# Performance work log

Measured on AMD Instinct MI355X. Metric: run time of the kernel, lower is better.

Reference implementation:

```python
import jax, jax.numpy as jnp
import numpy as np

DIM = 256
NUM_HEADS = 8
SCALE = (DIM // NUM_HEADS) ** (-0.5)
EPS = 1e-6


def channel_layernorm(x, w, b):
    # LayerNorm over channel dim (axis=1) per spatial location, as in source
    u = jnp.mean(x, axis=1, keepdims=True)
    s = jnp.mean((x - u) ** 2, axis=1, keepdims=True)
    xn = (x - u) / jnp.sqrt(s + EPS)
    return w[:, None, None] * xn + b[:, None, None]


def conv1x1(x, W, b):
    # x: [B,C,H,W], W: [O,C], b: [O]
    return jnp.einsum('bchw,oc->bohw', x, W) + b[:, None, None]


def setup_inputs() -> dict:
    key = jax.random.key(0)
    ks = jax.random.split(key, 10)
    B, C, H, W = 8, DIM, 48, 48
    inp = {
        'x1': jax.random.normal(ks[0], (B, C, H, W), jnp.float32),
        'x2': jax.random.normal(ks[1], (B, C, H, W), jnp.float32),
        'Wq': jax.random.normal(ks[2], (C, C), jnp.float32) * (1.0 / np.sqrt(C)),
        'bq': jnp.zeros((C,), jnp.float32),
        'Wk': jax.random.normal(ks[3], (C, C), jnp.float32) * (1.0 / np.sqrt(C)),
        'bk': jnp.zeros((C,), jnp.float32),
        'Wv': jax.random.normal(ks[4], (C, C), jnp.float32) * (1.0 / np.sqrt(C)),
        'bv': jnp.zeros((C,), jnp.float32),
        'Wp': jax.random.normal(ks[5], (C, C), jnp.float32) * (1.0 / np.sqrt(C)),
        'bp': jnp.zeros((C,), jnp.float32),
        'w_nq': jnp.ones((C,), jnp.float32),
        'b_nq': jnp.zeros((C,), jnp.float32),
        'w_nkv': jnp.ones((C,), jnp.float32),
        'b_nkv': jnp.zeros((C,), jnp.float32),
    }
    return inp


def reference(x1, x2, Wq, bq, Wk, bk, Wv, bv, Wp, bp, w_nq, b_nq, w_nkv, b_nkv):
    B, C, H, W = x1.shape
    x1n = channel_layernorm(x1, w_nq, b_nq)
    x2n = channel_layernorm(x2, w_nkv, b_nkv)
    # project then flatten spatial -> tokens: [B, N, C]
    q = conv1x1(x1n, Wq, bq).reshape(B, C, H * W).transpose(0, 2, 1)
    k = conv1x1(x2n, Wk, bk).reshape(B, C, H * W).transpose(0, 2, 1)
    v = conv1x1(x2n, Wv, bv).reshape(B, C, H * W).transpose(0, 2, 1)
    # single-head full attention over N tokens (heads never split in source)
    attn = jnp.einsum('bnc,bmc->bnm', q, k) * SCALE
    attn = jax.nn.softmax(attn, axis=-1)
    out = jnp.einsum('bnm,bmc->bnc', attn, v)  # [B,N,C]
    out = out.transpose(0, 2, 1).reshape(B, C, H, W)
    out = conv1x1(out, Wp, bp)
    return out + x1
```

## Files before the change

kernel.cpp:

```cpp
#include <hip/hip_runtime.h>

#define NB 8
#define CH 256
#define NT 2304
#define KVSPLIT 3
#define TPS 12
#define ATTN_SCALE 0.17677669529663687f
#define LN_EPS 1e-6f

typedef __attribute__((ext_vector_type(8))) short short8;
typedef __attribute__((ext_vector_type(4))) float f32x4;
typedef __attribute__((ext_vector_type(4))) unsigned short ushort4v;
typedef __attribute__((ext_vector_type(8))) unsigned short ushort8v;
typedef __attribute__((ext_vector_type(4))) float float4v;

__device__ __forceinline__ unsigned short f2bf(float f) {
  unsigned int u = __float_as_uint(f);
  u += 0x7fffu + ((u >> 16) & 1u);
  return (unsigned short)(u >> 16);
}
__device__ __forceinline__ float bf2f(unsigned short s) {
  return __uint_as_float(((unsigned int)s) << 16);
}

__device__ __forceinline__ void gload_lds16(const void* g, void* l) {
  __builtin_amdgcn_global_load_lds(
      (const __attribute__((address_space(1))) unsigned int*)g,
      (__attribute__((address_space(3))) unsigned int*)l, 16, 0, 0);
}

__global__ __launch_bounds__(256) void wconv_kernel(
    const float* __restrict__ wq, const float* __restrict__ wk,
    const float* __restrict__ wv, const float* __restrict__ wp,
    unsigned short* __restrict__ out) {
  int z = blockIdx.y;
  const float* src = (z == 0) ? wq : (z == 1) ? wk : (z == 2) ? wv : wp;
  unsigned short* dst = out + z * 65536;
  int i = (blockIdx.x * 256 + threadIdx.x) * 4;
  float4v v = *(const float4v*)(src + i);
  ushort4v r;
  r[0] = f2bf(v[0]); r[1] = f2bf(v[1]); r[2] = f2bf(v[2]); r[3] = f2bf(v[3]);
  *(ushort4v*)(dst + i) = r;
}

__global__ __launch_bounds__(256) void ln_kernel(
    const float* __restrict__ x1, const float* __restrict__ x2,
    const float* __restrict__ w1, const float* __restrict__ b1,
    const float* __restrict__ w2, const float* __restrict__ b2,
    unsigned short* __restrict__ o1, unsigned short* __restrict__ o2) {
  __shared__ float part[4][64][2];
  __shared__ float fin[64][2];
  int z = blockIdx.z;
  const float* x = z ? x2 : x1;
  const float* w = z ? w2 : w1;
  const float* bias = z ? b2 : b1;
  unsigned short* out = z ? o2 : o1;
  int tid = threadIdx.x;
  int lane = tid & 63, wv = tid >> 6;
  int n0 = blockIdx.x * 64;
  int b = blockIdx.y;
  const float* xp = x + (size_t)b * CH * NT + n0 + lane;
  float sum = 0.f, ss = 0.f;
#pragma unroll 4
  for (int c = wv * 64; c < wv * 64 + 64; ++c) {
    float v = xp[(size_t)c * NT];
    sum += v; ss += v * v;
  }
  part[wv][lane][0] = sum;
  part[wv][lane][1] = ss;
  __syncthreads();
  if (tid < 64) {
    float s = 0.f, q = 0.f;
#pragma unroll
    for (int wi = 0; wi < 4; ++wi) { s += part[wi][tid][0]; q += part[wi][tid][1]; }
    float u = s * (1.0f / CH);
    float var = q * (1.0f / CH) - u * u;
    fin[tid][0] = u;
    fin[tid][1] = rsqrtf(var + LN_EPS);
  }
  __syncthreads();
  float u = fin[lane][0], rstd = fin[lane][1];
  unsigned short* op = out + ((size_t)b * NT + n0 + lane) * CH;
  for (int c0 = wv * 64; c0 < wv * 64 + 64; c0 += 8) {
    ushort8v pk;
#pragma unroll
    for (int j = 0; j < 8; ++j) {
      float v = xp[(size_t)(c0 + j) * NT];
      pk[j] = f2bf((v - u) * rstd * w[c0 + j] + bias[c0 + j]);
    }
    *(ushort8v*)(op + c0) = pk;
  }
}

__global__ __launch_bounds__(256) void proj_kernel(
    const unsigned short* __restrict__ xq, const unsigned short* __restrict__ xkv,
    const unsigned short* __restrict__ wbf,
    const float* __restrict__ bq, const float* __restrict__ bk,
    const float* __restrict__ bv,
    unsigned short* __restrict__ q, unsigned short* __restrict__ k,
    unsigned short* __restrict__ vt) {
  __shared__ char As[16384];
  __shared__ char Bs[16384];
  int tid = threadIdx.x;
  int lane = tid & 63, wid = tid >> 6;
  int z = blockIdx.z;
  int b = z / 3, pz = z - b * 3;
  const unsigned short* A = ((pz == 0) ? xq : xkv) + (size_t)b * NT * CH;
  const unsigned short* W = wbf + pz * 65536;
  const float* bias = (pz == 0) ? bq : (pz == 1) ? bk : bv;
  int m0 = blockIdx.x * 128;
  int c0 = blockIdx.y * 128;
  int wr = wid >> 1, wc = wid & 1;

  f32x4 zero4 = {0.f, 0.f, 0.f, 0.f};
  f32x4 acc[4][4];
#pragma unroll
  for (int i = 0; i < 4; ++i)
#pragma unroll
    for (int j = 0; j < 4; ++j) acc[i][j] = zero4;

  for (int kt = 0; kt < 4; ++kt) {
#pragma unroll
    for (int it = 0; it < 4; ++it) {
      int li = it * 256 + tid;
      int X = li * 16;
      int row = X >> 7;
      int colb = (X & 127) ^ ((row & 7) << 4);
      gload_lds16((const char*)A + ((size_t)(m0 + row) * CH + kt * 64) * 2 + colb,
                  As + it * 4096 + wid * 1024);
      gload_lds16((const char*)W + ((size_t)(c0 + row) * CH + kt * 64) * 2 + colb,
                  Bs + it * 4096 + wid * 1024);
    }
    __syncthreads();
#pragma unroll
    for (int kk = 0; kk < 2; ++kk) {
      int cb = kk * 64 + ((lane >> 4) << 4);
      short8 af[4], bf[4];
#pragma unroll
      for (int mi = 0; mi < 4; ++mi) {
        int row = wr * 64 + mi * 16 + (lane & 15);
        af[mi] = *(const short8*)(As + row * 128 + (cb ^ ((row & 7) << 4)));
      }
#pragma unroll
      for (int ni = 0; ni < 4; ++ni) {
        int row = wc * 64 + ni * 16 + (lane & 15);
        bf[ni] = *(const short8*)(Bs + row * 128 + (cb ^ ((row & 7) << 4)));
      }
#pragma unroll
      for (int mi = 0; mi < 4; ++mi)
#pragma unroll
        for (int ni = 0; ni < 4; ++ni)
          acc[mi][ni] = __builtin_amdgcn_mfma_f32_16x16x32_bf16(
              af[mi], bf[ni], acc[mi][ni], 0, 0, 0);
    }
    __syncthreads();
  }

  int colbase = c0 + wc * 64;
  int rowbase = m0 + wr * 64;
  if (pz < 2) {
    unsigned short* dst = ((pz == 0) ? q : k) + (size_t)b * NT * CH;
#pragma unroll
    for (int mi = 0; mi < 4; ++mi)
#pragma unroll
      for (int ni = 0; ni < 4; ++ni) {
        int col = colbase + ni * 16 + (lane & 15);
        float bb = bias[col];
        int row0 = rowbase + mi * 16 + ((lane >> 4) << 2);
#pragma unroll
        for (int r = 0; r < 4; ++r)
          dst[(size_t)(row0 + r) * CH + col] = f2bf(acc[mi][ni][r] + bb);
      }
  } else {
    unsigned short* dst = vt + (size_t)b * CH * NT;
#pragma unroll
    for (int mi = 0; mi < 4; ++mi)
#pragma unroll
      for (int ni = 0; ni < 4; ++ni) {
        int col = colbase + ni * 16 + (lane & 15);
        float bb = bias[col];
        int row0 = rowbase + mi * 16 + ((lane >> 4) << 2);
        ushort4v pk;
#pragma unroll
        for (int r = 0; r < 4; ++r) pk[r] = f2bf(acc[mi][ni][r] + bb);
        *(ushort4v*)(dst + (size_t)col * NT + row0) = pk;
      }
  }
}

__global__ __launch_bounds__(256, 2) void attn_kernel(
    const unsigned short* __restrict__ q, const unsigned short* __restrict__ k,
    const unsigned short* __restrict__ vt,
    unsigned short* __restrict__ op0, unsigned short* __restrict__ op1,
    unsigned short* __restrict__ op2, float* __restrict__ ml) {
  __shared__ char Ks[2][32768];
  __shared__ char Ps[9216];
  __shared__ float Alf[64];
  int tid = threadIdx.x, lane = tid & 63, wid = tid >> 6;
  int b = blockIdx.z;
  int split = blockIdx.y;
  int q0 = blockIdx.x * 64;
  const unsigned short* qb = q + (size_t)b * NT * CH;
  const unsigned short* kb = k + (size_t)b * NT * CH;
  const unsigned short* vb = vt + (size_t)b * CH * NT;
  int hi = lane >> 4, lo = lane & 15;

  short8 qf[8];
  int qrow = q0 + wid * 16 + lo;
#pragma unroll
  for (int ks = 0; ks < 8; ++ks)
    qf[ks] = *(const short8*)(qb + (size_t)qrow * CH + ks * 32 + hi * 8);

  f32x4 zero4 = {0.f, 0.f, 0.f, 0.f};
  f32x4 o[16];
#pragma unroll
  for (int ci = 0; ci < 16; ++ci) o[ci] = zero4;
  float mrun = -INFINITY, lrun = 0.f;

  int kt0base = split * TPS * 64;
#pragma unroll
  for (int it = 0; it < 8; ++it) {
    int X = (it * 256 + tid) * 16;
    int row = X >> 9;
    int colb = (X & 511) ^ ((row & 7) << 4);
    gload_lds16((const char*)kb + ((size_t)(kt0base + row) * CH) * 2 + colb,
                Ks[0] + it * 4096 + wid * 1024);
  }
  __syncthreads();

  for (int t = 0; t < TPS; ++t) {
    int kt0 = kt0base + t * 64;
    int cur = t & 1;
    if (t + 1 < TPS) {
#pragma unroll
      for (int it = 0; it < 8; ++it) {
        int X = (it * 256 + tid) * 16;
        int row = X >> 9;
        int colb = (X & 511) ^ ((row & 7) << 4);
        gload_lds16((const char*)kb + ((size_t)(kt0 + 64 + row) * CH) * 2 + colb,
                    Ks[cur ^ 1] + it * 4096 + wid * 1024);
      }
    }
    short8 vf[8];
#pragma unroll
    for (int di = 0; di < 4; ++di)
#pragma unroll
      for (int ks2 = 0; ks2 < 2; ++ks2)
        vf[di * 2 + ks2] = *(const short8*)(
            vb + (size_t)(wid * 64 + di * 16 + lo) * NT + kt0 + ks2 * 32 + hi * 8);

    f32x4 s[4];
#pragma unroll
    for (int ct = 0; ct < 4; ++ct) s[ct] = zero4;
#pragma unroll
    for (int ct = 0; ct < 4; ++ct) {
      int row = ct * 16 + lo;
      const char* kp = Ks[cur] + row * 512;
      int swz = (row & 7) << 4;
#pragma unroll
      for (int ks = 0; ks < 8; ++ks) {
        short8 kf = *(const short8*)(kp + ((ks * 64 + hi * 16) ^ swz));
        s[ct] = __builtin_amdgcn_mfma_f32_16x16x32_bf16(kf, qf[ks], s[ct], 0, 0, 0);
      }
    }

    float mx = -INFINITY;
#pragma unroll
    for (int ct = 0; ct < 4; ++ct) {
      f32x4 sv = s[ct] * ATTN_SCALE;
      s[ct] = sv;
      mx = fmaxf(fmaxf(fmaxf(mx, sv[0]), fmaxf(sv[1], sv[2])), sv[3]);
    }
    mx = fmaxf(mx, __shfl_xor(mx, 16));
    mx = fmaxf(mx, __shfl_xor(mx, 32));
    float mnew = fmaxf(mrun, mx);
    float alpha = __expf(mrun - mnew);
    mrun = mnew;
    float rs = 0.f;
    unsigned short* prow = (unsigned short*)(Ps + (wid * 16 + lo) * 144 + hi * 8);
#pragma unroll
    for (int ct = 0; ct < 4; ++ct) {
      ushort4v pk;
#pragma unroll
      for (int r = 0; r < 4; ++r) {
        float p = __expf(s[ct][r] - mnew);
        rs += p;
        pk[r] = f2bf(p);
      }
      *(ushort4v*)(prow + ct * 16) = pk;
    }
    rs += __shfl_xor(rs, 16);
    rs += __shfl_xor(rs, 32);
    lrun = lrun * alpha + rs;
    if (lane < 16) Alf[wid * 16 + lane] = alpha;
    __syncthreads();

    f32x4 af[4];
#pragma unroll
    for (int qg = 0; qg < 4; ++qg)
      af[qg] = *(const f32x4*)(Alf + qg * 16 + hi * 4);
#pragma unroll
    for (int qg = 0; qg < 4; ++qg)
#pragma unroll
      for (int di = 0; di < 4; ++di) o[qg * 4 + di] *= af[qg];

#pragma unroll
    for (int ks2 = 0; ks2 < 2; ++ks2) {
      short8 pa[4];
#pragma unroll
      for (int qg = 0; qg < 4; ++qg)
        pa[qg] = *(const short8*)(Ps + (qg * 16 + lo) * 144 + ks2 * 64 + hi * 16);
#pragma unroll
      for (int di = 0; di < 4; ++di)
#pragma unroll
        for (int qg = 0; qg < 4; ++qg)
          o[qg * 4 + di] = __builtin_amdgcn_mfma_f32_16x16x32_bf16(
              pa[qg], vf[di * 2 + ks2], o[qg * 4 + di], 0, 0, 0);
    }
    __syncthreads();
  }

  unsigned short* od = ((split == 0) ? op0 : (split == 1) ? op1 : op2) +
                       ((size_t)b * NT + q0) * CH;
#pragma unroll
  for (int qg = 0; qg < 4; ++qg)
#pragma unroll
    for (int di = 0; di < 4; ++di) {
      int d = wid * 64 + di * 16 + lo;
#pragma unroll
      for (int r = 0; r < 4; ++r) {
        int qr = qg * 16 + hi * 4 + r;
        od[(size_t)qr * CH + d] = f2bf(o[qg * 4 + di][r]);
      }
    }
  float* mlp = ml + ((size_t)(split * NB + b) * NT + q0) * 2;
  if (lane < 16) {
    int qr = wid * 16 + lane;
    mlp[qr * 2] = mrun;
    mlp[qr * 2 + 1] = lrun;
  }
}

__global__ __launch_bounds__(256) void combine_kernel(
    const unsigned short* __restrict__ op0, const unsigned short* __restrict__ op1,
    const unsigned short* __restrict__ op2, const float* __restrict__ ml,
    unsigned short* __restrict__ oa) {
  int g = blockIdx.x;
  int d = threadIdx.x;
  const size_t S = (size_t)NB * NT;
  float m0 = ml[(size_t)g * 2], l0 = ml[(size_t)g * 2 + 1];
  float m1 = ml[(S + g) * 2], l1 = ml[(S + g) * 2 + 1];
  float m2 = ml[(2 * S + g) * 2], l2 = ml[(2 * S + g) * 2 + 1];
  float M = fmaxf(fmaxf(m0, m1), m2);
  float w0 = __expf(m0 - M), w1 = __expf(m1 - M), w2 = __expf(m2 - M);
  float L = w0 * l0 + w1 * l1 + w2 * l2;
  float o0 = bf2f(op0[(size_t)g * CH + d]);
  float o1 = bf2f(op1[(size_t)g * CH + d]);
  float o2 = bf2f(op2[(size_t)g * CH + d]);
  oa[(size_t)g * CH + d] = f2bf((w0 * o0 + w1 * o1 + w2 * o2) / L);
}

__global__ __launch_bounds__(256) void oproj_kernel(
    const unsigned short* __restrict__ oa, const unsigned short* __restrict__ wp,
    const float* __restrict__ bp, const float* __restrict__ x1,
    float* __restrict__ outp) {
  __shared__ char As[16384];
  __shared__ char Bs[16384];
  int tid = threadIdx.x;
  int lane = tid & 63, wid = tid >> 6;
  int b = blockIdx.z;
  const unsigned short* A = oa + (size_t)b * NT * CH;
  int m0 = blockIdx.x * 128;
  int c0 = blockIdx.y * 128;
  int wr = wid >> 1, wc = wid & 1;

  f32x4 zero4 = {0.f, 0.f, 0.f, 0.f};
  f32x4 acc[4][4];
#pragma unroll
  for (int i = 0; i < 4; ++i)
#pragma unroll
    for (int j = 0; j < 4; ++j) acc[i][j] = zero4;

  for (int kt = 0; kt < 4; ++kt) {
#pragma unroll
    for (int it = 0; it < 4; ++it) {
      int li = it * 256 + tid;
      int X = li * 16;
      int row = X >> 7;
      int colb = (X & 127) ^ ((row & 7) << 4);
      gload_lds16((const char*)A + ((size_t)(m0 + row) * CH + kt * 64) * 2 + colb,
                  As + it * 4096 + wid * 1024);
      gload_lds16((const char*)wp + ((size_t)(c0 + row) * CH + kt * 64) * 2 + colb,
                  Bs + it * 4096 + wid * 1024);
    }
    __syncthreads();
#pragma unroll
    for (int kk = 0; kk < 2; ++kk) {
      int cb = kk * 64 + ((lane >> 4) << 4);
      short8 af[4], bf[4];
#pragma unroll
      for (int mi = 0; mi < 4; ++mi) {
        int row = wr * 64 + mi * 16 + (lane & 15);
        af[mi] = *(const short8*)(As + row * 128 + (cb ^ ((row & 7) << 4)));
      }
#pragma unroll
      for (int ni = 0; ni < 4; ++ni) {
        int row = wc * 64 + ni * 16 + (lane & 15);
        bf[ni] = *(const short8*)(Bs + row * 128 + (cb ^ ((row & 7) << 4)));
      }
#pragma unroll
      for (int mi = 0; mi < 4; ++mi)
#pragma unroll
        for (int ni = 0; ni < 4; ++ni)
          acc[mi][ni] = __builtin_amdgcn_mfma_f32_16x16x32_bf16(
              af[mi], bf[ni], acc[mi][ni], 0, 0, 0);
    }
    __syncthreads();
  }

  int colbase = c0 + wc * 64;
  int rowbase = m0 + wr * 64;
#pragma unroll
  for (int mi = 0; mi < 4; ++mi)
#pragma unroll
    for (int ni = 0; ni < 4; ++ni) {
      int col = colbase + ni * 16 + (lane & 15);
      float bb = bp[col];
      int row0 = rowbase + mi * 16 + ((lane >> 4) << 2);
      int base = (b * CH + col) * NT + row0;
      float4v xv = *(const float4v*)(x1 + base);
      float4v rs;
#pragma unroll
      for (int r = 0; r < 4; ++r) rs[r] = acc[mi][ni][r] + bb + xv[r];
      *(float4v*)(outp + base) = rs;
    }
}

extern "C" void kernel_launch(void* const* d_in, const int* in_sizes, int n_in,
                              void* d_out, int out_size, void* d_ws, size_t ws_size,
                              hipStream_t stream) {
  (void)in_sizes; (void)n_in; (void)out_size; (void)ws_size;
  const float* x1 = (const float*)d_in[0];
  const float* x2 = (const float*)d_in[1];
  const float* Wq = (const float*)d_in[2];
  const float* bq = (const float*)d_in[3];
  const float* Wk = (const float*)d_in[4];
  const float* bk = (const float*)d_in[5];
  const float* Wv = (const float*)d_in[6];
  const float* bv = (const float*)d_in[7];
  const float* Wp = (const float*)d_in[8];
  const float* bp = (const float*)d_in[9];
  const float* wnq = (const float*)d_in[10];
  const float* bnq = (const float*)d_in[11];
  const float* wnkv = (const float*)d_in[12];
  const float* bnkv = (const float*)d_in[13];
  float* outp = (float*)d_out;

  const size_t TSZ = (size_t)NB * NT * CH;
  unsigned short* xq = (unsigned short*)d_ws;
  unsigned short* xkv = xq + TSZ;
  unsigned short* qb = xkv + TSZ;
  unsigned short* kbuf = qb + TSZ;
  unsigned short* vtb = kbuf + TSZ;
  unsigned short* oab = vtb + TSZ;
  unsigned short* wbf = oab + TSZ;
  float* ml = (float*)(wbf + 4 * 65536);

  wconv_kernel<<<dim3(64, 4), dim3(256), 0, stream>>>(Wq, Wk, Wv, Wp, wbf);
  ln_kernel<<<dim3(36, 8, 2), dim3(256), 0, stream>>>(x1, x2, wnq, bnq, wnkv, bnkv,
                                                      xq, xkv);
  proj_kernel<<<dim3(18, 2, 24), dim3(256), 0, stream>>>(xq, xkv, wbf, bq, bk, bv,
                                                         qb, kbuf, vtb);
  attn_kernel<<<dim3(36, KVSPLIT, 8), dim3(256), 0, stream>>>(qb, kbuf, vtb,
                                                              xq, xkv, oab, ml);
  combine_kernel<<<dim3(NB * NT), dim3(256), 0, stream>>>(xq, xkv, oab, ml, oab);
  oproj_kernel<<<dim3(18, 2, 8), dim3(256), 0, stream>>>(oab, wbf + 3 * 65536, bp,
                                                         x1, outp);
}
```

Before: 158.4 us.

## Rewrite attention with 32x32 MFMA, register-resident P, lazy rescale, vectorized combine

The attention kernel now handles 128 queries per block, with each wave owning 32 query rows. It uses 32x32x16 bf16 MFMA and keeps the softmax probabilities in registers, converted with v_cvt_pk_bf16_f32, so the LDS P buffer and the alpha-exchange barrier are gone. The attention scale moves into the Q projection, and the running-max rescale only happens when the max grows by more than 8, which relies on bf16/fp32 headroom. The LN kernel also caches the input column in registers instead of reading x twice, and the combine kernel is vectorized to 8 elements per thread with a precomputed reciprocal. The cost is higher register pressure in attention, and the deferred max may reduce accuracy.

Result: slower. 316.3 us (+99.7%).

```diff
diff --git a/kernel.cpp b/kernel.cpp
--- a/kernel.cpp
+++ b/kernel.cpp
@@ -5,11 +5,13 @@
 #define NT 2304
 #define KVSPLIT 3
 #define TPS 12
+#define QB 128
 #define ATTN_SCALE 0.17677669529663687f
 #define LN_EPS 1e-6f
 
 typedef __attribute__((ext_vector_type(8))) short short8;
 typedef __attribute__((ext_vector_type(4))) float f32x4;
+typedef __attribute__((ext_vector_type(16))) float f32x16;
 typedef __attribute__((ext_vector_type(4))) unsigned short ushort4v;
 typedef __attribute__((ext_vector_type(8))) unsigned short ushort8v;
 typedef __attribute__((ext_vector_type(4))) float float4v;
@@ -21,6 +23,11 @@
 }
 __device__ __forceinline__ float bf2f(unsigned short s) {
   return __uint_as_float(((unsigned int)s) << 16);
+}
+__device__ __forceinline__ unsigned int cvtpk(float a, float b) {
+  unsigned int r;
+  asm("v_cvt_pk_bf16_f32 %0, %1, %2" : "=v"(r) : "v"(a), "v"(b));
+  return r;
 }
 
 __device__ __forceinline__ void gload_lds16(const void* g, void* l) {
@@ -60,10 +67,12 @@
   int n0 = blockIdx.x * 64;
   int b = blockIdx.y;
   const float* xp = x + (size_t)b * CH * NT + n0 + lane;
+  float xc[64];
   float sum = 0.f, ss = 0.f;
-#pragma unroll 4
-  for (int c = wv * 64; c < wv * 64 + 64; ++c) {
-    float v = xp[(size_t)c * NT];
+#pragma unroll
+  for (int j = 0; j < 64; ++j) {
+    float v = xp[(size_t)(wv * 64 + j) * NT];
+    xc[j] = v;
     sum += v; ss += v * v;
   }
   part[wv][lane][0] = sum;
@@ -81,14 +90,14 @@
   __syncthreads();
   float u = fin[lane][0], rstd = fin[lane][1];
   unsigned short* op = out + ((size_t)b * NT + n0 + lane) * CH;
-  for (int c0 = wv * 64; c0 < wv * 64 + 64; c0 += 8) {
+#pragma unroll
+  for (int c0 = 0; c0 < 64; c0 += 8) {
     ushort8v pk;
 #pragma unroll
-    for (int j = 0; j < 8; ++j) {
-      float v = xp[(size_t)(c0 + j) * NT];
-      pk[j] = f2bf((v - u) * rstd * w[c0 + j] + bias[c0 + j]);
-    }
-    *(ushort8v*)(op + c0) = pk;
+    for (int j = 0; j < 8; ++j)
+      pk[j] = f2bf((xc[c0 + j] - u) * rstd * w[wv * 64 + c0 + j] +
+                   bias[wv * 64 + c0 + j]);
+    *(ushort8v*)(op + wv * 64 + c0) = pk;
   }
 }
 
@@ -160,6 +169,7 @@
   int rowbase = m0 + wr * 64;
   if (pz < 2) {
     unsigned short* dst = ((pz == 0) ? q : k) + (size_t)b * NT * CH;
+    float scl = (pz == 0) ? ATTN_SCALE : 1.0f;
 #pragma unroll
     for (int mi = 0; mi < 4; ++mi)
 #pragma unroll
@@ -169,7 +179,7 @@
         int row0 = rowbase + mi * 16 + ((lane >> 4) << 2);
 #pragma unroll
         for (int r = 0; r < 4; ++r)
-          dst[(size_t)(row0 + r) * CH + col] = f2bf(acc[mi][ni][r] + bb);
+          dst[(size_t)(row0 + r) * CH + col] = f2bf((acc[mi][ni][r] + bb) * scl);
       }
   } else {
     unsigned short* dst = vt + (size_t)b * CH * NT;
@@ -194,27 +204,24 @@
     unsigned short* __restrict__ op0, unsigned short* __restrict__ op1,
     unsigned short* __restrict__ op2, float* __restrict__ ml) {
   __shared__ char Ks[2][32768];
-  __shared__ char Ps[9216];
-  __shared__ float Alf[64];
   int tid = threadIdx.x, lane = tid & 63, wid = tid >> 6;
+  int r31 = lane & 31, h2 = lane >> 5;
   int b = blockIdx.z;
   int split = blockIdx.y;
-  int q0 = blockIdx.x * 64;
-  const unsigned short* qb = q + (size_t)b * NT * CH;
+  int q0 = blockIdx.x * QB;
+  const unsigned short* qb_ = q + (size_t)b * NT * CH;
   const unsigned short* kb = k + (size_t)b * NT * CH;
-  const unsigned short* vb = vt + (size_t)b * CH * NT;
-  int hi = lane >> 4, lo = lane & 15;
-
-  short8 qf[8];
-  int qrow = q0 + wid * 16 + lo;
-#pragma unroll
-  for (int ks = 0; ks < 8; ++ks)
-    qf[ks] = *(const short8*)(qb + (size_t)qrow * CH + ks * 32 + hi * 8);
-
-  f32x4 zero4 = {0.f, 0.f, 0.f, 0.f};
-  f32x4 o[16];
-#pragma unroll
-  for (int ci = 0; ci < 16; ++ci) o[ci] = zero4;
+  const unsigned short* vbase = vt + (size_t)b * CH * NT + (size_t)r31 * NT;
+
+  int qrow = q0 + wid * 32 + r31;
+  short8 qf[16];
+#pragma unroll
+  for (int st = 0; st < 16; ++st)
+    qf[st] = *(const short8*)(qb_ + (size_t)qrow * CH + st * 16 + h2 * 8);
+
+  f32x16 o[8];
+#pragma unroll
+  for (int i = 0; i < 8; ++i) o[i] = (f32x16){};
   float mrun = -INFINITY, lrun = 0.f;
 
   int kt0base = split * TPS * 64;
@@ -228,9 +235,12 @@
   }
   __syncthreads();
 
+  union V8 { struct { ushort4v a, b; } h; short8 s8; };
+  union PB { unsigned int u[4]; short8 s8; };
+
   for (int t = 0; t < TPS; ++t) {
     int kt0 = kt0base + t * 64;
-    int cur = t & 1;
+    const char* kbase = Ks[t & 1];
     if (t + 1 < TPS) {
 #pragma unroll
       for (int it = 0; it < 8; ++it) {
@@ -238,106 +248,106 @@
         int row = X >> 9;
         int colb = (X & 511) ^ ((row & 7) << 4);
         gload_lds16((const char*)kb + ((size_t)(kt0 + 64 + row) * CH) * 2 + colb,
-                    Ks[cur ^ 1] + it * 4096 + wid * 1024);
-      }
-    }
-    short8 vf[8];
-#pragma unroll
-    for (int di = 0; di < 4; ++di)
-#pragma unroll
-      for (int ks2 = 0; ks2 < 2; ++ks2)
-        vf[di * 2 + ks2] = *(const short8*)(
-            vb + (size_t)(wid * 64 + di * 16 + lo) * NT + kt0 + ks2 * 32 + hi * 8);
-
-    f32x4 s[4];
-#pragma unroll
-    for (int ct = 0; ct < 4; ++ct) s[ct] = zero4;
-#pragma unroll
-    for (int ct = 0; ct < 4; ++ct) {
-      int row = ct * 16 + lo;
-      const char* kp = Ks[cur] + row * 512;
-      int swz = (row & 7) << 4;
-#pragma unroll
-      for (int ks = 0; ks < 8; ++ks) {
-        short8 kf = *(const short8*)(kp + ((ks * 64 + hi * 16) ^ swz));
-        s[ct] = __builtin_amdgcn_mfma_f32_16x16x32_bf16(kf, qf[ks], s[ct], 0, 0, 0);
-      }
-    }
+                    Ks[(t + 1) & 1] + it * 4096 + wid * 1024);
+      }
+    }
+
+    f32x16 s0 = (f32x16){}, s1 = (f32x16){};
+    __builtin_amdgcn_s_setprio(1);
+#pragma unroll
+    for (int st = 0; st < 16; ++st) {
+      int cb = (st * 32 + h2 * 16);
+      short8 kf0 = *(const short8*)(kbase + r31 * 512 + (cb ^ ((r31 & 7) << 4)));
+      s0 = __builtin_amdgcn_mfma_f32_32x32x16_bf16(kf0, qf[st], s0, 0, 0, 0);
+      int row1 = 32 + r31;
+      short8 kf1 = *(const short8*)(kbase + row1 * 512 + (cb ^ ((row1 & 7) << 4)));
+      s1 = __builtin_amdgcn_mfma_f32_32x32x16_bf16(kf1, qf[st], s1, 0, 0, 0);
+    }
+    __builtin_amdgcn_s_setprio(0);
 
     float mx = -INFINITY;
 #pragma unroll
-    for (int ct = 0; ct < 4; ++ct) {
-      f32x4 sv = s[ct] * ATTN_SCALE;
-      s[ct] = sv;
-      mx = fmaxf(fmaxf(fmaxf(mx, sv[0]), fmaxf(sv[1], sv[2])), sv[3]);
-    }
-    mx = fmaxf(mx, __shfl_xor(mx, 16));
+    for (int i = 0; i < 16; ++i) mx = fmaxf(mx, fmaxf(s0[i], s1[i]));
     mx = fmaxf(mx, __shfl_xor(mx, 32));
-    float mnew = fmaxf(mrun, mx);
-    float alpha = __expf(mrun - mnew);
-    mrun = mnew;
+    if (__any(mx - mrun > 8.0f)) {
+      float mnew = fmaxf(mrun, mx);
+      float al = __expf(mrun - mnew);
+      lrun *= al;
+      mrun = mnew;
+#pragma unroll
+      for (int i = 0; i < 8; ++i) o[i] = o[i] * al;
+    }
     float rs = 0.f;
-    unsigned short* prow = (unsigned short*)(Ps + (wid * 16 + lo) * 144 + hi * 8);
-#pragma unroll
-    for (int ct = 0; ct < 4; ++ct) {
+#pragma unroll
+    for (int i = 0; i < 16; ++i) {
+      s0[i] = __expf(s0[i] - mrun); rs += s0[i];
+      s1[i] = __expf(s1[i] - mrun); rs += s1[i];
+    }
+    rs += __shfl_xor(rs, 32);
+    lrun += rs;
+
+    PB pb00, pb01, pb10, pb11;
+    pb00.u[0] = cvtpk(s0[0], s0[1]);   pb00.u[1] = cvtpk(s0[2], s0[3]);
+    pb00.u[2] = cvtpk(s0[4], s0[5]);   pb00.u[3] = cvtpk(s0[6], s0[7]);
+    pb01.u[0] = cvtpk(s0[8], s0[9]);   pb01.u[1] = cvtpk(s0[10], s0[11]);
+    pb01.u[2] = cvtpk(s0[12], s0[13]); pb01.u[3] = cvtpk(s0[14], s0[15]);
+    pb10.u[0] = cvtpk(s1[0], s1[1]);   pb10.u[1] = cvtpk(s1[2], s1[3]);
+    pb10.u[2] = cvtpk(s1[4], s1[5]);   pb10.u[3] = cvtpk(s1[6], s1[7]);
+    pb11.u[0] = cvtpk(s1[8], s1[9]);   pb11.u[1] = cvtpk(s1[10], s1[11]);
+    pb11.u[2] = cvtpk(s1[12], s1[13]); pb11.u[3] = cvtpk(s1[14], s1[15]);
+
+#define LOADV(dst, d2)                                                         \
+    {                                                                          \
+      const unsigned short* vr = vbase + (size_t)((d2) * 32) * NT + kt0;       \
+      dst[0].h.a = *(const ushort4v*)(vr + 4 * h2);                            \
+      dst[0].h.b = *(const ushort4v*)(vr + 4 * h2 + 8);                        \
+      dst[1].h.a = *(const ushort4v*)(vr + 16 + 4 * h2);                       \
+      dst[1].h.b = *(const ushort4v*)(vr + 16 + 4 * h2 + 8);                   \
+      dst[2].h.a = *(const ushort4v*)(vr + 32 + 4 * h2);                       \
+      dst[2].h.b = *(const ushort4v*)(vr + 32 + 4 * h2 + 8);                   \
+      dst[3].h.a = *(const ushort4v*)(vr + 48 + 4 * h2);                       \
+      dst[3].h.b = *(const ushort4v*)(vr + 48 + 4 * h2 + 8);                   \
+    }
+#define MFMA4(v, d2)                                                           \
+    {                                                                          \
+      o[d2] = __builtin_amdgcn_mfma_f32_32x32x16_bf16(v[0].s8, pb00.s8, o[d2], 0, 0, 0); \
+      o[d2] = __builtin_amdgcn_mfma_f32_32x32x16_bf16(v[1].s8, pb01.s8, o[d2], 0, 0, 0); \
+      o[d2] = __builtin_amdgcn_mfma_f32_32x32x16_bf16(v[2].s8, pb10.s8, o[d2], 0, 0, 0); \
+      o[d2] = __builtin_amdgcn_mfma_f32_32x32x16_bf16(v[3].s8, pb11.s8, o[d2], 0, 0, 0); \
+    }
+    {
+      V8 va[4], vb2[4];
+      LOADV(va, 0);
+#pragma unroll
+      for (int d2 = 0; d2 < 8; d2 += 2) {
+        LOADV(vb2, d2 + 1);
+        __builtin_amdgcn_s_setprio(1);
+        MFMA4(va, d2);
+        __builtin_amdgcn_s_setprio(0);
+        if (d2 < 6) LOADV(va, d2 + 2);
+        __builtin_amdgcn_s_setprio(1);
+        MFMA4(vb2, d2 + 1);
+        __builtin_amdgcn_s_setprio(0);
+      }
+    }
+    __syncthreads();
+  }
+
+  unsigned short* od = ((split == 0) ? op0 : (split == 1) ? op1 : op2) +
+                       (size_t)(b * NT + qrow) * CH;
+#pragma unroll
+  for (int d2 = 0; d2 < 8; ++d2)
+#pragma unroll
+    for (int m = 0; m < 4; ++m) {
       ushort4v pk;
 #pragma unroll
-      for (int r = 0; r < 4; ++r) {
-        float p = __expf(s[ct][r] - mnew);
-        rs += p;
-        pk[r] = f2bf(p);
-      }
-      *(ushort4v*)(prow + ct * 16) = pk;
-    }
-    rs += __shfl_xor(rs, 16);
-    rs += __shfl_xor(rs, 32);
-    lrun = lrun * alpha + rs;
-    if (lane < 16) Alf[wid * 16 + lane] = alpha;
-    __syncthreads();
-
-    f32x4 af[4];
-#pragma unroll
-    for (int qg = 0; qg < 4; ++qg)
-      af[qg] = *(const f32x4*)(Alf + qg * 16 + hi * 4);
-#pragma unroll
-    for (int qg = 0; qg < 4; ++qg)
-#pragma unroll
-      for (int di = 0; di < 4; ++di) o[qg * 4 + di] *= af[qg];
-
-#pragma unroll
-    for (int ks2 = 0; ks2 < 2; ++ks2) {
-      short8 pa[4];
-#pragma unroll
-      for (int qg = 0; qg < 4; ++qg)
-        pa[qg] = *(const short8*)(Ps + (qg * 16 + lo) * 144 + ks2 * 64 + hi * 16);
-#pragma unroll
-      for (int di = 0; di < 4; ++di)
-#pragma unroll
-        for (int qg = 0; qg < 4; ++qg)
-          o[qg * 4 + di] = __builtin_amdgcn_mfma_f32_16x16x32_bf16(
-              pa[qg], vf[di * 2 + ks2], o[qg * 4 + di], 0, 0, 0);
-    }
-    __syncthreads();
-  }
-
-  unsigned short* od = ((split == 0) ? op0 : (split == 1) ? op1 : op2) +
-                       ((size_t)b * NT + q0) * CH;
-#pragma unroll
-  for (int qg = 0; qg < 4; ++qg)
-#pragma unroll
-    for (int di = 0; di < 4; ++di) {
-      int d = wid * 64 + di * 16 + lo;
-#pragma unroll
-      for (int r = 0; r < 4; ++r) {
-        int qr = qg * 16 + hi * 4 + r;
-        od[(size_t)qr * CH + d] = f2bf(o[qg * 4 + di][r]);
-      }
-    }
-  float* mlp = ml + ((size_t)(split * NB + b) * NT + q0) * 2;
-  if (lane < 16) {
-    int qr = wid * 16 + lane;
-    mlp[qr * 2] = mrun;
-    mlp[qr * 2 + 1] = lrun;
+      for (int r = 0; r < 4; ++r) pk[r] = f2bf(o[d2][m * 4 + r]);
+      *(ushort4v*)(od + d2 * 32 + m * 8 + h2 * 4) = pk;
+    }
+  if (lane < 32) {
+    float* mlp = ml + ((size_t)(split * NB + b) * NT + q0 + wid * 32 + lane) * 2;
+    mlp[0] = mrun;
+    mlp[1] = lrun;
   }
 }
 
@@ -345,19 +355,24 @@
     const unsigned short* __restrict__ op0, const unsigned short* __restrict__ op1,
     const unsigned short* __restrict__ op2, const float* __restrict__ ml,
     unsigned short* __restrict__ oa) {
-  int g = blockIdx.x;
-  int d = threadIdx.x;
   const size_t S = (size_t)NB * NT;
+  int g = blockIdx.x * 8 + (threadIdx.x >> 5);
+  int c = (threadIdx.x & 31) * 8;
   float m0 = ml[(size_t)g * 2], l0 = ml[(size_t)g * 2 + 1];
   float m1 = ml[(S + g) * 2], l1 = ml[(S + g) * 2 + 1];
   float m2 = ml[(2 * S + g) * 2], l2 = ml[(2 * S + g) * 2 + 1];
   float M = fmaxf(fmaxf(m0, m1), m2);
   float w0 = __expf(m0 - M), w1 = __expf(m1 - M), w2 = __expf(m2 - M);
-  float L = w0 * l0 + w1 * l1 + w2 * l2;
-  float o0 = bf2f(op0[(size_t)g * CH + d]);
-  float o1 = bf2f(op1[(size_t)g * CH + d]);
-  float o2 = bf2f(op2[(size_t)g * CH + d]);
-  oa[(size_t)g * CH + d] = f2bf((w0 * o0 + w1 * o1 + w2 * o2) / L);
+  float Li = 1.0f / (w0 * l0 + w1 * l1 + w2 * l2);
+  w0 *= Li; w1 *= Li; w2 *= Li;
+  ushort8v a0 = *(const ushort8v*)(op0 + (size_t)g * CH + c);
+  ushort8v a1 = *(const ushort8v*)(op1 + (size_t)g * CH + c);
+  ushort8v a2 = *(const ushort8v*)(op2 + (size_t)g * CH + c);
+  ushort8v r;
+#pragma unroll
+  for (int j = 0; j < 8; ++j)
+    r[j] = f2bf(w0 * bf2f(a0[j]) + w1 * bf2f(a1[j]) + w2 * bf2f(a2[j]));
+  *(ushort8v*)(oa + (size_t)g * CH + c) = r;
 }
 
 __global__ __launch_bounds__(256) void oproj_kernel(
@@ -471,9 +486,10 @@
                                                       xq, xkv);
   proj_kernel<<<dim3(18, 2, 24), dim3(256), 0, stream>>>(xq, xkv, wbf, bq, bk, bv,
                                                          qb, kbuf, vtb);
-  attn_kernel<<<dim3(36, KVSPLIT, 8), dim3(256), 0, stream>>>(qb, kbuf, vtb,
-                                                              xq, xkv, oab, ml);
-  combine_kernel<<<dim3(NB * NT), dim3(256), 0, stream>>>(xq, xkv, oab, ml, oab);
+  attn_kernel<<<dim3(NT / QB, KVSPLIT, 8), dim3(256), 0, stream>>>(
+      qb, kbuf, vtb, xq, xkv, oab, ml);
+  combine_kernel<<<dim3(NB * NT / 8), dim3(256), 0, stream>>>(xq, xkv, oab, ml,
+                                                              oab);
   oproj_kernel<<<dim3(18, 2, 8), dim3(256), 0, stream>>>(oab, wbf + 3 * 65536, bp,
                                                          x1, outp);
 }
```
